# Optimization experiments

Measured on AMD Instinct MI355X. Metric: run time of the kernel, lower is better.

Reference implementation:

```python
import jax, jax.numpy as jnp
import numpy as np

D_MODEL = 1024
N_HEAD = 16
D_K = D_MODEL // N_HEAD


def setup_inputs() -> dict:
    key = jax.random.key(0)
    ks = jax.random.split(key, 9)
    s = 1.0 / np.sqrt(D_MODEL)
    return {
        "x": jax.random.normal(ks[0], (2, 2048, D_MODEL), dtype=jnp.float32),
        "Wq": jax.random.uniform(ks[1], (D_MODEL, D_MODEL), jnp.float32, -s, s),
        "bq": jax.random.uniform(ks[2], (D_MODEL,), jnp.float32, -s, s),
        "Wk": jax.random.uniform(ks[3], (D_MODEL, D_MODEL), jnp.float32, -s, s),
        "bk": jax.random.uniform(ks[4], (D_MODEL,), jnp.float32, -s, s),
        "Wv": jax.random.uniform(ks[5], (D_MODEL, D_MODEL), jnp.float32, -s, s),
        "bv": jax.random.uniform(ks[6], (D_MODEL,), jnp.float32, -s, s),
        "Wo": jax.random.uniform(ks[7], (D_MODEL, D_MODEL), jnp.float32, -s, s),
        "bo": jax.random.uniform(ks[8], (D_MODEL,), jnp.float32, -s, s),
    }


def reference(x, Wq, bq, Wk, bk, Wv, bv, Wo, bo):
    B, S, D = x.shape
    # linear projections (torch Linear: x @ W.T + b)
    q = x @ Wq.T + bq
    k = x @ Wk.T + bk
    v = x @ Wv.T + bv
    # split heads: [B, H, S, d_k]
    q = q.reshape(B, S, N_HEAD, D_K).transpose(0, 2, 1, 3)
    k = k.reshape(B, S, N_HEAD, D_K).transpose(0, 2, 1, 3)
    v = v.reshape(B, S, N_HEAD, D_K).transpose(0, 2, 1, 3)
    scores = jnp.einsum("bhqd,bhkd->bhqk", q, k) / np.sqrt(D_K).astype(jnp.float32)
    attn = jax.nn.softmax(scores, axis=-1)
    out = jnp.einsum("bhqk,bhkd->bhqd", attn, v)
    out = out.transpose(0, 2, 1, 3).reshape(B, S, D)
    return out @ Wo.T + bo
```

## Files before the change

kernel.cpp:

```cpp
#include <hip/hip_runtime.h>
#include <hip/hip_bf16.h>


typedef unsigned short u16;
typedef __attribute__((ext_vector_type(4))) unsigned short u16x4;
typedef __attribute__((ext_vector_type(8))) short short8;
typedef __attribute__((ext_vector_type(4))) float f32x4;

__device__ __forceinline__ u16 f2bf(float f) {
  __bf16 b = (__bf16)f;
  return __builtin_bit_cast(unsigned short, b);
}

__device__ __forceinline__ f32x4 mfma_bf16(short8 a, short8 b, f32x4 c) {
  return __builtin_amdgcn_mfma_f32_16x16x32_bf16(a, b, c, 0, 0, 0);
}

#define GLL16(gp, lp) __builtin_amdgcn_global_load_lds( \
    (const __attribute__((address_space(1))) void*)(gp), \
    (__attribute__((address_space(3))) void*)(lp), 16, 0, 0)

#define QSCALE 0.18033688011112042f

__global__ __launch_bounds__(256) void cast_all(
    const float* __restrict__ x,
    const float* __restrict__ wq, const float* __restrict__ wk,
    const float* __restrict__ wv, const float* __restrict__ wo,
    u16* __restrict__ xb, u16* __restrict__ wqb, u16* __restrict__ wkb,
    u16* __restrict__ wvb, u16* __restrict__ wob)
{
  const int z = blockIdx.z;
  const float* s; u16* d; int n4;
  if (z == 0)      { s = x;  d = xb;  n4 = 1048576; }
  else if (z == 1) { s = wq; d = wqb; n4 = 262144; }
  else if (z == 2) { s = wk; d = wkb; n4 = 262144; }
  else if (z == 3) { s = wv; d = wvb; n4 = 262144; }
  else             { s = wo; d = wob; n4 = 262144; }
  int i = blockIdx.x * 256 + threadIdx.x;
  if (i >= n4) return;
  float4 v = ((const float4*)s)[i];
  u16x4 o; o[0] = f2bf(v.x); o[1] = f2bf(v.y); o[2] = f2bf(v.z); o[3] = f2bf(v.w);
  ((u16x4*)d)[i] = o;
}

__device__ __forceinline__ void gemm_core(const u16* __restrict__ A,
                                          const u16* __restrict__ B,
                                          u16* sA, u16* sB, f32x4 acc[4][4])
{
  const int tid = threadIdx.x;
  const int lane = tid & 63, wave = tid >> 6;
  const int wr = wave >> 1, wc = wave & 1;
  const int m0 = blockIdx.y * 128, n0 = blockIdx.x * 128;
  const u16* ga = A + (size_t)(m0 + (tid >> 2)) * 1024 + (tid & 3) * 8;
  const u16* gb = B + (size_t)(n0 + (tid >> 2)) * 1024 + (tid & 3) * 8;
  u16* la0 = sA + wave * 512;          u16* la1 = sA + 2048 + wave * 512;
  u16* lb0 = sB + wave * 512;          u16* lb1 = sB + 2048 + wave * 512;
  const int rl = lane & 15, kg = (lane >> 4) * 8;

  for (int k0 = 0; k0 < 1024; k0 += 32) {
    GLL16(ga + k0,             la0);
    GLL16(ga + 64 * 1024 + k0, la1);
    GLL16(gb + k0,             lb0);
    GLL16(gb + 64 * 1024 + k0, lb1);
    __syncthreads();
    short8 af[4], bf_[4];
#pragma unroll
    for (int m = 0; m < 4; ++m) af[m]  = *(const short8*)&sA[(wr * 64 + m * 16 + rl) * 32 + kg];
#pragma unroll
    for (int n = 0; n < 4; ++n) bf_[n] = *(const short8*)&sB[(wc * 64 + n * 16 + rl) * 32 + kg];
#pragma unroll
    for (int m = 0; m < 4; ++m)
#pragma unroll
      for (int n = 0; n < 4; ++n)
        acc[m][n] = mfma_bf16(af[m], bf_[n], acc[m][n]);
    __syncthreads();
  }
}

__global__ __launch_bounds__(256) void gemm_qkv(
    const u16* __restrict__ X,
    const u16* __restrict__ Wqb, const u16* __restrict__ Wkb, const u16* __restrict__ Wvb,
    const float* __restrict__ bq, const float* __restrict__ bk, const float* __restrict__ bv,
    u16* __restrict__ Qo, u16* __restrict__ Ko, u16* __restrict__ Vt)
{
  __shared__ u16 sA[4096], sB[4096];
  const int z = blockIdx.z;
  const u16* W = (z == 0) ? Wqb : (z == 1) ? Wkb : Wvb;
  const float* bias = (z == 0) ? bq : (z == 1) ? bk : bv;

  f32x4 acc[4][4];
#pragma unroll
  for (int m = 0; m < 4; ++m)
#pragma unroll
    for (int n = 0; n < 4; ++n) acc[m][n] = (f32x4){0.f, 0.f, 0.f, 0.f};

  gemm_core(X, W, sA, sB, acc);

  const int lane = threadIdx.x & 63, wave = threadIdx.x >> 6;
  const int wr = wave >> 1, wc = wave & 1;
  const int m0 = blockIdx.y * 128, n0 = blockIdx.x * 128;
  const int rl = lane & 15, rg = (lane >> 4) * 4;

  if (z < 2) {
    u16* dst = (z == 0) ? Qo : Ko;
    const float cs = (z == 0) ? QSCALE : 1.0f;
#pragma unroll
    for (int n = 0; n < 4; ++n) {
      int col = n0 + wc * 64 + n * 16 + rl;
      float bb = bias[col];
#pragma unroll
      for (int m = 0; m < 4; ++m) {
        int row0 = m0 + wr * 64 + m * 16 + rg;
#pragma unroll
        for (int r = 0; r < 4; ++r)
          dst[(size_t)(row0 + r) * 1024 + col] = f2bf((acc[m][n][r] + bb) * cs);
      }
    }
  } else {
#pragma unroll
    for (int n = 0; n < 4; ++n) {
      int col = n0 + wc * 64 + n * 16 + rl;
      float bb = bias[col];
#pragma unroll
      for (int m = 0; m < 4; ++m) {
        int row0 = m0 + wr * 64 + m * 16 + rg;
        int bidx = row0 >> 11, sl = row0 & 2047;
        u16x4 pk;
#pragma unroll
        for (int r = 0; r < 4; ++r) pk[r] = f2bf(acc[m][n][r] + bb);
        *(u16x4*)&Vt[((size_t)(bidx * 1024 + col)) * 2048 + sl] = pk;
      }
    }
  }
}

__global__ __launch_bounds__(256) void gemm_out(
    const u16* __restrict__ Ob, const u16* __restrict__ Wob,
    const float* __restrict__ bo, float* __restrict__ Out)
{
  __shared__ u16 sA[4096], sB[4096];
  f32x4 acc[4][4];
#pragma unroll
  for (int m = 0; m < 4; ++m)
#pragma unroll
    for (int n = 0; n < 4; ++n) acc[m][n] = (f32x4){0.f, 0.f, 0.f, 0.f};

  gemm_core(Ob, Wob, sA, sB, acc);

  const int lane = threadIdx.x & 63, wave = threadIdx.x >> 6;
  const int wr = wave >> 1, wc = wave & 1;
  const int m0 = blockIdx.y * 128, n0 = blockIdx.x * 128;
  const int rl = lane & 15, rg = (lane >> 4) * 4;
#pragma unroll
  for (int n = 0; n < 4; ++n) {
    int col = n0 + wc * 64 + n * 16 + rl;
    float bb = bo[col];
#pragma unroll
    for (int m = 0; m < 4; ++m) {
      int row0 = m0 + wr * 64 + m * 16 + rg;
#pragma unroll
      for (int r = 0; r < 4; ++r)
        Out[(size_t)(row0 + r) * 1024 + col] = acc[m][n][r] + bb;
    }
  }
}

__global__ __launch_bounds__(512) void attn_fwd(
    const u16* __restrict__ Q, const u16* __restrict__ K,
    const u16* __restrict__ Vt, u16* __restrict__ O)
{
  __shared__ u16 sK[2][64][64];
  __shared__ u16 sV[2][64][64];

  const int tid = threadIdx.x, lane = tid & 63, wave = tid >> 6;
  const int rl = lane & 15, g = lane >> 4;

  const int bflat = blockIdx.x;
  const int xcd = bflat & 7, j = bflat >> 3;
  const int bh = xcd * 4 + (j >> 4);
  const int qchunk = j & 15;
  const int b = bh >> 4, h = bh & 15;
  const int qbase = qchunk * 128 + wave * 16;

  const u16* Qp = Q + (size_t)(b * 2048 + qbase) * 1024 + h * 64;
  const u16* Kp = K + (size_t)(b * 2048) * 1024 + h * 64;
  const u16* Vp = Vt + (size_t)(bh * 64) * 2048;

  short8 qf[2];
#pragma unroll
  for (int hf = 0; hf < 2; ++hf)
    qf[hf] = *(const short8*)&Qp[(size_t)rl * 1024 + hf * 32 + g * 8];

  const int keyperm = 8 * (rl >> 2) + (rl & 3);
  const int swzK8 = (((rl & 3) | (((rl >> 2) & 1) << 2))) * 8;
  const int swzV8 = (rl & 7) * 8;

  const int srow = lane >> 3;
  const int feK = (((lane & 7) ^ (srow & 3)) * 8) ^ ((wave & 1) * 32);
  const int feV = (((lane & 7) ^ srow) * 8);

  f32x4 oacc[4];
  f32x4 lacc = (f32x4){0.f, 0.f, 0.f, 0.f};
#pragma unroll
  for (int dg = 0; dg < 4; ++dg) oacc[dg] = (f32x4){0.f, 0.f, 0.f, 0.f};
  float mrun = -INFINITY;

  const short8 ONES = {0x3F80, 0x3F80, 0x3F80, 0x3F80,
                       0x3F80, 0x3F80, 0x3F80, 0x3F80};

  auto stage = [&](int nb, int kt) {
    const int grow = wave * 8 + srow;
    GLL16(Kp + (size_t)(kt + grow) * 1024 + feK, &sK[nb][wave * 8][0]);
    GLL16(Vp + (size_t)grow * 2048 + kt + feV,   &sV[nb][wave * 8][0]);
  };

  auto proc_sub = [&](int nb, int sub) {
    short8 kf[2][2];
#pragma unroll
    for (int t = 0; t < 2; ++t) {
      const int r = sub * 32 + keyperm + 4 * t;
#pragma unroll
      for (int hf = 0; hf < 2; ++hf)
        kf[t][hf] = *(const short8*)&sK[nb][r][(hf * 32 + g * 8) ^ swzK8];
    }
    short8 vf[4];
#pragma unroll
    for (int dg = 0; dg < 4; ++dg)
      vf[dg] = *(const short8*)&sV[nb][dg * 16 + rl][(sub * 32 + g * 8) ^ swzV8];

    f32x4 sc[2];
    __builtin_amdgcn_s_setprio(1);
#pragma unroll
    for (int t = 0; t < 2; ++t) {
      f32x4 a = (f32x4){0.f, 0.f, 0.f, 0.f};
      a = mfma_bf16(kf[t][0], qf[0], a);
      a = mfma_bf16(kf[t][1], qf[1], a);
      sc[t] = a;
    }
    __builtin_amdgcn_s_setprio(0);

    float p2[8];
#pragma unroll
    for (int t = 0; t < 2; ++t)
#pragma unroll
      for (int r = 0; r < 4; ++r) p2[t * 4 + r] = sc[t][r];
    float a0 = fmaxf(fmaxf(p2[0], p2[1]), p2[2]);
    float a1 = fmaxf(fmaxf(p2[3], p2[4]), p2[5]);
    float a2 = fmaxf(p2[6], p2[7]);
    float tm = fmaxf(fmaxf(a0, a1), a2);
    if (!__all(tm <= mrun + 8.0f)) {
      tm = fmaxf(tm, __shfl_xor(tm, 16));
      tm = fmaxf(tm, __shfl_xor(tm, 32));
      float mnew = fmaxf(mrun, tm);
      float sfac = __builtin_amdgcn_exp2f(mrun - mnew);
      mrun = mnew;
#pragma unroll
      for (int dg = 0; dg < 4; ++dg)
#pragma unroll
        for (int r = 0; r < 4; ++r) oacc[dg][r] *= sfac;
      lacc[0] *= sfac;
    }
    short8 pb;
#pragma unroll
    for (int j2 = 0; j2 < 8; ++j2)
      pb[j2] = (short)f2bf(__builtin_amdgcn_exp2f(p2[j2] - mrun));

    __builtin_amdgcn_s_setprio(1);
    lacc = mfma_bf16(ONES, pb, lacc);
#pragma unroll
    for (int dg = 0; dg < 4; ++dg)
      oacc[dg] = mfma_bf16(vf[dg], pb, oacc[dg]);
    __builtin_amdgcn_s_setprio(0);
  };

  stage(0, 0);
  __syncthreads();
  for (int kt = 0; kt < 2048; kt += 128) {
    stage(1, kt + 64);
    proc_sub(0, 0);
    proc_sub(0, 1);
    __syncthreads();
    if (kt + 128 < 2048) stage(0, kt + 128);
    proc_sub(1, 0);
    proc_sub(1, 1);
    __syncthreads();
  }

  float inv = 1.0f / lacc[0];
  int qrow = qbase + rl;
  u16* op = O + (size_t)(b * 2048 + qrow) * 1024 + h * 64;
#pragma unroll
  for (int dg = 0; dg < 4; ++dg) {
    u16x4 pk;
#pragma unroll
    for (int r = 0; r < 4; ++r) pk[r] = f2bf(oacc[dg][r] * inv);
    *(u16x4*)&op[dg * 16 + g * 4] = pk;
  }
}

extern "C" void kernel_launch(void* const* d_in, const int* in_sizes, int n_in,
                              void* d_out, int out_size, void* d_ws, size_t ws_size,
                              hipStream_t stream) {
  const float* x  = (const float*)d_in[0];
  const float* Wq = (const float*)d_in[1];
  const float* bq = (const float*)d_in[2];
  const float* Wk = (const float*)d_in[3];
  const float* bk = (const float*)d_in[4];
  const float* Wv = (const float*)d_in[5];
  const float* bv = (const float*)d_in[6];
  const float* Wo = (const float*)d_in[7];
  const float* bo = (const float*)d_in[8];

  char* ws = (char*)d_ws;
  const size_t MB = 1024 * 1024;
  u16* Xb  = (u16*)(ws + 0 * MB);
  u16* Wqb = (u16*)(ws + 8 * MB);
  u16* Wkb = (u16*)(ws + 10 * MB);
  u16* Wvb = (u16*)(ws + 12 * MB);
  u16* Wob = (u16*)(ws + 14 * MB);
  u16* Qb  = (u16*)(ws + 16 * MB);
  u16* Kb  = (u16*)(ws + 24 * MB);
  u16* Vtb = (u16*)(ws + 32 * MB);
  u16* Ob  = (u16*)(ws + 40 * MB);

  cast_all<<<dim3(4096, 1, 5), 256, 0, stream>>>(x, Wq, Wk, Wv, Wo,
                                                 Xb, Wqb, Wkb, Wvb, Wob);
  gemm_qkv<<<dim3(8, 32, 3), 256, 0, stream>>>(Xb, Wqb, Wkb, Wvb,
                                               bq, bk, bv, Qb, Kb, Vtb);
  attn_fwd<<<dim3(512), 512, 0, stream>>>(Qb, Kb, Vtb, Ob);
  gemm_out<<<dim3(8, 32), 256, 0, stream>>>(Ob, Wob, bo, (float*)d_out);
}
```

Measured before the change: 117.0 us.

## Double-buffer GEMM LDS tiles to overlap global loads with MFMA

Converts the shared GEMM core from single-buffered to double-buffered LDS staging. The next k-tile is issued with global_load_lds while the current tile is computed, and explicit vmcnt waits and barriers replace the two syncthreads per iteration. This targets the load latency exposed at each k-step in the QKV and output projections. In exchange it doubles LDS per block to 32KB, which may lower occupancy, and relies on hand-written waitcnt ordering.

```diff
diff --git a/kernel.cpp b/kernel.cpp
--- a/kernel.cpp
+++ b/kernel.cpp
@@ -19,6 +19,10 @@
 #define GLL16(gp, lp) __builtin_amdgcn_global_load_lds( \
     (const __attribute__((address_space(1))) void*)(gp), \
     (__attribute__((address_space(3))) void*)(lp), 16, 0, 0)
+
+#define WAITV4 asm volatile("s_waitcnt vmcnt(4)" ::: "memory")
+#define WAITV0 asm volatile("s_waitcnt vmcnt(0)" ::: "memory")
+#define BAR __builtin_amdgcn_s_barrier()
 
 #define QSCALE 0.18033688011112042f
 
@@ -53,28 +57,41 @@
   const int m0 = blockIdx.y * 128, n0 = blockIdx.x * 128;
   const u16* ga = A + (size_t)(m0 + (tid >> 2)) * 1024 + (tid & 3) * 8;
   const u16* gb = B + (size_t)(n0 + (tid >> 2)) * 1024 + (tid & 3) * 8;
-  u16* la0 = sA + wave * 512;          u16* la1 = sA + 2048 + wave * 512;
-  u16* lb0 = sB + wave * 512;          u16* lb1 = sB + 2048 + wave * 512;
+  const int lofs = wave * 512;
   const int rl = lane & 15, kg = (lane >> 4) * 8;
 
-  for (int k0 = 0; k0 < 1024; k0 += 32) {
-    GLL16(ga + k0,             la0);
-    GLL16(ga + 64 * 1024 + k0, la1);
-    GLL16(gb + k0,             lb0);
-    GLL16(gb + 64 * 1024 + k0, lb1);
-    __syncthreads();
+  auto stage = [&](int nb, int k0) {
+    GLL16(ga + k0,             sA + nb * 4096 + lofs);
+    GLL16(ga + 64 * 1024 + k0, sA + nb * 4096 + 2048 + lofs);
+    GLL16(gb + k0,             sB + nb * 4096 + lofs);
+    GLL16(gb + 64 * 1024 + k0, sB + nb * 4096 + 2048 + lofs);
+  };
+
+  auto compute = [&](int nb) {
+    const u16* bA = sA + nb * 4096;
+    const u16* bB = sB + nb * 4096;
     short8 af[4], bf_[4];
 #pragma unroll
-    for (int m = 0; m < 4; ++m) af[m]  = *(const short8*)&sA[(wr * 64 + m * 16 + rl) * 32 + kg];
-#pragma unroll
-    for (int n = 0; n < 4; ++n) bf_[n] = *(const short8*)&sB[(wc * 64 + n * 16 + rl) * 32 + kg];
+    for (int m = 0; m < 4; ++m) af[m]  = *(const short8*)&bA[(wr * 64 + m * 16 + rl) * 32 + kg];
+#pragma unroll
+    for (int n = 0; n < 4; ++n) bf_[n] = *(const short8*)&bB[(wc * 64 + n * 16 + rl) * 32 + kg];
 #pragma unroll
     for (int m = 0; m < 4; ++m)
 #pragma unroll
       for (int n = 0; n < 4; ++n)
         acc[m][n] = mfma_bf16(af[m], bf_[n], acc[m][n]);
-    __syncthreads();
-  }
+  };
+
+  stage(0, 0);
+#pragma unroll 1
+  for (int t = 0; t < 31; ++t) {
+    stage((t + 1) & 1, (t + 1) * 32);
+    WAITV4; BAR;
+    compute(t & 1);
+    BAR;
+  }
+  WAITV0; BAR;
+  compute(1);
 }
 
 __global__ __launch_bounds__(256) void gemm_qkv(
@@ -83,7 +100,7 @@
     const float* __restrict__ bq, const float* __restrict__ bk, const float* __restrict__ bv,
     u16* __restrict__ Qo, u16* __restrict__ Ko, u16* __restrict__ Vt)
 {
-  __shared__ u16 sA[4096], sB[4096];
+  __shared__ u16 sA[8192], sB[8192];
   const int z = blockIdx.z;
   const u16* W = (z == 0) ? Wqb : (z == 1) ? Wkb : Wvb;
   const float* bias = (z == 0) ? bq : (z == 1) ? bk : bv;
@@ -138,7 +155,7 @@
     const u16* __restrict__ Ob, const u16* __restrict__ Wob,
     const float* __restrict__ bo, float* __restrict__ Out)
 {
-  __shared__ u16 sA[4096], sB[4096];
+  __shared__ u16 sA[8192], sB[8192];
   f32x4 acc[4][4];
 #pragma unroll
   for (int m = 0; m < 4; ++m)
```

New measurement: 126.8 us. +8.4%, slower.

## Double GEMM K-tile to 64 and XOR-swizzle LDS layout to avoid bank conflicts

Applied to the files above, without the earlier changes.

The shared GEMM core now loads a 64-wide K slice per iteration instead of 32, halving the number of barrier pairs and global-load rounds across the K loop. The LDS layout uses an XOR swizzle of 16-byte slots by row, applied both when filling via global_load_lds and when reading fragments, to reduce bank conflicts on the 128-byte row stride. LDS usage per block doubles to 32 KB, which may reduce occupancy.

```diff
diff --git a/kernel.cpp b/kernel.cpp
--- a/kernel.cpp
+++ b/kernel.cpp
@@ -51,28 +51,37 @@
   const int lane = tid & 63, wave = tid >> 6;
   const int wr = wave >> 1, wc = wave & 1;
   const int m0 = blockIdx.y * 128, n0 = blockIdx.x * 128;
-  const u16* ga = A + (size_t)(m0 + (tid >> 2)) * 1024 + (tid & 3) * 8;
-  const u16* gb = B + (size_t)(n0 + (tid >> 2)) * 1024 + (tid & 3) * 8;
-  u16* la0 = sA + wave * 512;          u16* la1 = sA + 2048 + wave * 512;
-  u16* lb0 = sB + wave * 512;          u16* lb1 = sB + 2048 + wave * 512;
-  const int rl = lane & 15, kg = (lane >> 4) * 8;
-
-  for (int k0 = 0; k0 < 1024; k0 += 32) {
-    GLL16(ga + k0,             la0);
-    GLL16(ga + 64 * 1024 + k0, la1);
-    GLL16(gb + k0,             lb0);
-    GLL16(gb + 64 * 1024 + k0, lb1);
+  const int lr = lane >> 3;
+  const int gslot = ((lane & 7) ^ lr) * 8;
+  const u16* ga = A + (size_t)(m0 + lr) * 1024 + gslot;
+  const u16* gb = B + (size_t)(n0 + lr) * 1024 + gslot;
+  const int rl = lane & 15, g = lane >> 4;
+  const int rsw = rl & 7;
+
+  for (int k0 = 0; k0 < 1024; k0 += 64) {
+#pragma unroll
+    for (int i = 0; i < 4; ++i) {
+      const int rowb = (wave * 4 + i) * 8;
+      GLL16(ga + (size_t)rowb * 1024 + k0, sA + rowb * 64);
+      GLL16(gb + (size_t)rowb * 1024 + k0, sB + rowb * 64);
+    }
     __syncthreads();
-    short8 af[4], bf_[4];
-#pragma unroll
-    for (int m = 0; m < 4; ++m) af[m]  = *(const short8*)&sA[(wr * 64 + m * 16 + rl) * 32 + kg];
-#pragma unroll
-    for (int n = 0; n < 4; ++n) bf_[n] = *(const short8*)&sB[(wc * 64 + n * 16 + rl) * 32 + kg];
-#pragma unroll
-    for (int m = 0; m < 4; ++m)
+#pragma unroll
+    for (int h = 0; h < 2; ++h) {
+      const int slot = ((h * 4 + g) ^ rsw) * 8;
+      short8 af[4], bf_[4];
+#pragma unroll
+      for (int m = 0; m < 4; ++m)
+        af[m]  = *(const short8*)&sA[(wr * 64 + m * 16 + rl) * 64 + slot];
 #pragma unroll
       for (int n = 0; n < 4; ++n)
-        acc[m][n] = mfma_bf16(af[m], bf_[n], acc[m][n]);
+        bf_[n] = *(const short8*)&sB[(wc * 64 + n * 16 + rl) * 64 + slot];
+#pragma unroll
+      for (int m = 0; m < 4; ++m)
+#pragma unroll
+        for (int n = 0; n < 4; ++n)
+          acc[m][n] = mfma_bf16(af[m], bf_[n], acc[m][n]);
+    }
     __syncthreads();
   }
 }
@@ -83,7 +92,7 @@
     const float* __restrict__ bq, const float* __restrict__ bk, const float* __restrict__ bv,
     u16* __restrict__ Qo, u16* __restrict__ Ko, u16* __restrict__ Vt)
 {
-  __shared__ u16 sA[4096], sB[4096];
+  __shared__ u16 sA[8192], sB[8192];
   const int z = blockIdx.z;
   const u16* W = (z == 0) ? Wqb : (z == 1) ? Wkb : Wvb;
   const float* bias = (z == 0) ? bq : (z == 1) ? bk : bv;
@@ -138,7 +147,7 @@
     const u16* __restrict__ Ob, const u16* __restrict__ Wob,
     const float* __restrict__ bo, float* __restrict__ Out)
 {
-  __shared__ u16 sA[4096], sB[4096];
+  __shared__ u16 sA[8192], sB[8192];
   f32x4 acc[4][4];
 #pragma unroll
   for (int m = 0; m < 4; ++m)
```

Result: slower. 124.3 us (+6.3%).

## Remap GEMM blocks per XCD and shrink out-projection tile to 64 rows

Applied to the files above, without the earlier changes.

The QKV GEMM now runs on a flat 1D grid that treats Wq/Wk/Wv as one contiguous 3072-row weight matrix. Block indices are remapped so each XCD (bflat&7) handles a contiguous band of M rows, which should improve L2 reuse of the X tiles. The output projection uses 64x128 tiles with 512 blocks instead of 256, filling more CUs. This relies on the three bf16 weight buffers being laid out back-to-back in the workspace, and the smaller tile does less MFMA work per LDS load.

```diff
diff --git a/kernel.cpp b/kernel.cpp
--- a/kernel.cpp
+++ b/kernel.cpp
@@ -45,12 +45,12 @@
 
 __device__ __forceinline__ void gemm_core(const u16* __restrict__ A,
                                           const u16* __restrict__ B,
+                                          int m0, int n0,
                                           u16* sA, u16* sB, f32x4 acc[4][4])
 {
   const int tid = threadIdx.x;
   const int lane = tid & 63, wave = tid >> 6;
   const int wr = wave >> 1, wc = wave & 1;
-  const int m0 = blockIdx.y * 128, n0 = blockIdx.x * 128;
   const u16* ga = A + (size_t)(m0 + (tid >> 2)) * 1024 + (tid & 3) * 8;
   const u16* gb = B + (size_t)(n0 + (tid >> 2)) * 1024 + (tid & 3) * 8;
   u16* la0 = sA + wave * 512;          u16* la1 = sA + 2048 + wave * 512;
@@ -78,14 +78,17 @@
 }
 
 __global__ __launch_bounds__(256) void gemm_qkv(
-    const u16* __restrict__ X,
-    const u16* __restrict__ Wqb, const u16* __restrict__ Wkb, const u16* __restrict__ Wvb,
+    const u16* __restrict__ X, const u16* __restrict__ Wqkv,
     const float* __restrict__ bq, const float* __restrict__ bk, const float* __restrict__ bv,
     u16* __restrict__ Qo, u16* __restrict__ Ko, u16* __restrict__ Vt)
 {
   __shared__ u16 sA[4096], sB[4096];
-  const int z = blockIdx.z;
-  const u16* W = (z == 0) ? Wqb : (z == 1) ? Wkb : Wvb;
+  const int bflat = blockIdx.x;
+  const int xcd = bflat & 7, idx = bflat >> 3;
+  const int m0 = (xcd * 4 + (idx & 3)) * 128;
+  const int nt = idx >> 2;
+  const int z = nt >> 3;
+  const int n0 = (nt & 7) * 128;
   const float* bias = (z == 0) ? bq : (z == 1) ? bk : bv;
 
   f32x4 acc[4][4];
@@ -94,11 +97,10 @@
 #pragma unroll
     for (int n = 0; n < 4; ++n) acc[m][n] = (f32x4){0.f, 0.f, 0.f, 0.f};
 
-  gemm_core(X, W, sA, sB, acc);
+  gemm_core(X, Wqkv, m0, nt * 128, sA, sB, acc);
 
   const int lane = threadIdx.x & 63, wave = threadIdx.x >> 6;
   const int wr = wave >> 1, wc = wave & 1;
-  const int m0 = blockIdx.y * 128, n0 = blockIdx.x * 128;
   const int rl = lane & 15, rg = (lane >> 4) * 4;
 
   if (z < 2) {
@@ -138,26 +140,51 @@
     const u16* __restrict__ Ob, const u16* __restrict__ Wob,
     const float* __restrict__ bo, float* __restrict__ Out)
 {
-  __shared__ u16 sA[4096], sB[4096];
-  f32x4 acc[4][4];
-#pragma unroll
-  for (int m = 0; m < 4; ++m)
+  __shared__ u16 sA[2048], sB[4096];
+  const int bflat = blockIdx.x;
+  const int xcd = bflat & 7, idx = bflat >> 3;
+  const int m0 = (xcd * 8 + (idx & 7)) * 64;
+  const int n0 = (idx >> 3) * 128;
+
+  const int tid = threadIdx.x, lane = tid & 63, wave = tid >> 6;
+  const int wr = wave >> 1, wc = wave & 1;
+  const u16* ga = Ob  + (size_t)(m0 + (tid >> 2)) * 1024 + (tid & 3) * 8;
+  const u16* gb = Wob + (size_t)(n0 + (tid >> 2)) * 1024 + (tid & 3) * 8;
+  u16* la0 = sA + wave * 512;
+  u16* lb0 = sB + wave * 512;          u16* lb1 = sB + 2048 + wave * 512;
+  const int rl = lane & 15, kg = (lane >> 4) * 8, rg = (lane >> 4) * 4;
+
+  f32x4 acc[2][4];
+#pragma unroll
+  for (int m = 0; m < 2; ++m)
 #pragma unroll
     for (int n = 0; n < 4; ++n) acc[m][n] = (f32x4){0.f, 0.f, 0.f, 0.f};
 
-  gemm_core(Ob, Wob, sA, sB, acc);
-
-  const int lane = threadIdx.x & 63, wave = threadIdx.x >> 6;
-  const int wr = wave >> 1, wc = wave & 1;
-  const int m0 = blockIdx.y * 128, n0 = blockIdx.x * 128;
-  const int rl = lane & 15, rg = (lane >> 4) * 4;
+  for (int k0 = 0; k0 < 1024; k0 += 32) {
+    GLL16(ga + k0,             la0);
+    GLL16(gb + k0,             lb0);
+    GLL16(gb + 64 * 1024 + k0, lb1);
+    __syncthreads();
+    short8 af[2], bf_[4];
+#pragma unroll
+    for (int m = 0; m < 2; ++m) af[m]  = *(const short8*)&sA[(wr * 32 + m * 16 + rl) * 32 + kg];
+#pragma unroll
+    for (int n = 0; n < 4; ++n) bf_[n] = *(const short8*)&sB[(wc * 64 + n * 16 + rl) * 32 + kg];
+#pragma unroll
+    for (int m = 0; m < 2; ++m)
+#pragma unroll
+      for (int n = 0; n < 4; ++n)
+        acc[m][n] = mfma_bf16(af[m], bf_[n], acc[m][n]);
+    __syncthreads();
+  }
+
 #pragma unroll
   for (int n = 0; n < 4; ++n) {
     int col = n0 + wc * 64 + n * 16 + rl;
     float bb = bo[col];
 #pragma unroll
-    for (int m = 0; m < 4; ++m) {
-      int row0 = m0 + wr * 64 + m * 16 + rg;
+    for (int m = 0; m < 2; ++m) {
+      int row0 = m0 + wr * 32 + m * 16 + rg;
 #pragma unroll
       for (int r = 0; r < 4; ++r)
         Out[(size_t)(row0 + r) * 1024 + col] = acc[m][n][r] + bb;
@@ -325,8 +352,7 @@
 
   cast_all<<<dim3(4096, 1, 5), 256, 0, stream>>>(x, Wq, Wk, Wv, Wo,
                                                  Xb, Wqb, Wkb, Wvb, Wob);
-  gemm_qkv<<<dim3(8, 32, 3), 256, 0, stream>>>(Xb, Wqb, Wkb, Wvb,
-                                               bq, bk, bv, Qb, Kb, Vtb);
+  gemm_qkv<<<dim3(768), 256, 0, stream>>>(Xb, Wqb, bq, bk, bv, Qb, Kb, Vtb);
   attn_fwd<<<dim3(512), 512, 0, stream>>>(Qb, Kb, Vtb, Ob);
-  gemm_out<<<dim3(8, 32), 256, 0, stream>>>(Ob, Wob, bo, (float*)d_out);
-}
+  gemm_out<<<dim3(512), 256, 0, stream>>>(Ob, Wob, bo, (float*)d_out);
+}
```

Result: slower. 121.6 us (+3.9%).
